# Kernel tuning notes

Measured on AMD Instinct MI355X. Metric: run time of the kernel, lower is better.

Reference implementation:

```python
import jax, jax.numpy as jnp
import numpy as np

N = 50000      # nodes
E = 600000     # edges (avg degree 12)
IN, H, OUT = 128, 256, 256


def setup_inputs() -> dict:
    key = jax.random.key(0)
    ks = jax.random.split(key, 9)
    glorot = lambda k, shp: jax.random.uniform(
        k, shp, jnp.float32, -1.0, 1.0) * np.sqrt(6.0 / (shp[0] + shp[1]))
    return {
        "x": jax.random.normal(ks[0], (N, IN), jnp.float32),
        "src": jax.random.randint(ks[1], (E,), 0, N, jnp.int32),
        "dst": jax.random.randint(ks[2], (E,), 0, N, jnp.int32),
        "W_conv": glorot(ks[3], (IN, H)),
        "b_conv": jnp.zeros((H,), jnp.float32),
        "W_fc": glorot(ks[4], (H, H)),
        "b_fc": jax.random.uniform(ks[5], (H,), jnp.float32, -1, 1) / np.sqrt(H),
        "W_fc2": glorot(ks[6], (H, OUT)),
        "b_fc2": jax.random.uniform(ks[7], (OUT,), jnp.float32, -1, 1) / np.sqrt(OUT),
    }


def reference(x, src, dst, W_conv, b_conv, W_fc, b_fc, W_fc2, b_fc2):
    ones = jnp.ones((E,), x.dtype)
    # dgl GraphConv, norm='both': D_in^{-1/2} A D_out^{-1/2} X W + b
    deg_out = jax.ops.segment_sum(ones, src, num_segments=N)
    deg_in = jax.ops.segment_sum(ones, dst, num_segments=N)
    norm_src = jax.lax.rsqrt(jnp.maximum(deg_out, 1.0))  # [N]
    norm_dst = jax.lax.rsqrt(jnp.maximum(deg_in, 1.0))   # [N]
    feat = x * norm_src[:, None]                          # [N, IN]
    agg = jax.ops.segment_sum(feat[src], dst, num_segments=N)  # gather+scatter SpMM
    h = agg * norm_dst[:, None]
    h = h @ W_conv + b_conv                               # GraphConv weight+bias
    # num_nonl_layers == 2 branch
    h = jax.nn.relu(h) @ W_fc + b_fc
    h = jax.nn.relu(h) @ W_fc2 + b_fc2
    return h
```

## Files before the change

kernel.cpp:

```cpp
#include <hip/hip_runtime.h>

#define NN 50000
#define NE 600000
#define FIN 128
#define CAP 128

typedef __attribute__((ext_vector_type(8))) short bf16x8;
typedef __attribute__((ext_vector_type(4))) float f32x4;

__device__ __forceinline__ float bf2f(unsigned short u) {
    union { unsigned int i; float f; } v; v.i = ((unsigned int)u) << 16; return v.f;
}
__device__ __forceinline__ unsigned short f2bf(float f) {
    union { float f; unsigned int i; } v; v.f = f;
    return (unsigned short)((v.i + 0x7FFFu + ((v.i >> 16) & 1u)) >> 16);
}

__global__ __launch_bounds__(256)
void bin_kernel(const int* __restrict__ src, const int* __restrict__ dst,
                int* __restrict__ cnt_in, int* __restrict__ cnt_out,
                int* __restrict__ csr_src) {
    int e0 = (blockIdx.x * 256 + threadIdx.x) * 4;
    if (e0 >= NE) return;
    int4 s4 = *(const int4*)(src + e0);
    int4 d4 = *(const int4*)(dst + e0);
    int p;
    p = atomicAdd(&cnt_in[d4.x], 1); if (p < CAP) csr_src[d4.x * CAP + p] = s4.x;
    atomicAdd(&cnt_out[s4.x], 1);
    p = atomicAdd(&cnt_in[d4.y], 1); if (p < CAP) csr_src[d4.y * CAP + p] = s4.y;
    atomicAdd(&cnt_out[s4.y], 1);
    p = atomicAdd(&cnt_in[d4.z], 1); if (p < CAP) csr_src[d4.z * CAP + p] = s4.z;
    atomicAdd(&cnt_out[s4.z], 1);
    p = atomicAdd(&cnt_in[d4.w], 1); if (p < CAP) csr_src[d4.w * CAP + p] = s4.w;
    atomicAdd(&cnt_out[s4.w], 1);
}

__global__ __launch_bounds__(256)
void gather_kernel(const float* __restrict__ x, const int* __restrict__ csr_src,
                   const int* __restrict__ cnt_in, const int* __restrict__ cnt_out,
                   unsigned short* __restrict__ agg) {
    int tid  = threadIdx.x;
    int grp  = tid >> 5;
    int lane = tid & 31;
    int r = blockIdx.x * 8 + grp;
    if (r >= NN) return;
    int deg = cnt_in[r];
    float nd = rsqrtf(fmaxf((float)deg, 1.0f));
    int cnt = deg > CAP ? CAP : deg;
    const int* bucket = csr_src + (size_t)r * CAP;
    const float* xb = x + lane * 4;
    float4 acc = {0.f, 0.f, 0.f, 0.f};
    for (int j0 = 0; j0 < cnt; j0 += 32) {
        int c = cnt - j0; if (c > 32) c = 32;
        int sv = 0; float nsl = 0.f;
        if (lane < c) {
            sv  = bucket[j0 + lane];
            nsl = rsqrtf(fmaxf((float)cnt_out[sv], 1.0f));
        }
        for (int i = 0; i < c; ++i) {
            int   s  = __shfl(sv,  i, 32);
            float ns = __shfl(nsl, i, 32);
            float4 xv = *(const float4*)(xb + (size_t)s * FIN);
            acc.x += xv.x * ns; acc.y += xv.y * ns;
            acc.z += xv.z * ns; acc.w += xv.w * ns;
        }
    }
    unsigned short o[4];
    o[0] = f2bf(acc.x * nd); o[1] = f2bf(acc.y * nd);
    o[2] = f2bf(acc.z * nd); o[3] = f2bf(acc.w * nd);
    *(uint2*)(agg + (size_t)r * FIN + lane * 4) = *(const uint2*)o;
}

template<int K, bool RELU>
__global__ __launch_bounds__(256)
void gemm_kernel(const unsigned short* __restrict__ A,
                 const float* __restrict__ W, const float* __restrict__ bias,
                 unsigned short* __restrict__ Cb, float* __restrict__ Cf, int ML) {
    const int PITCH = K + 24;
    __shared__ short bsh[64 * PITCH];
    int tid  = threadIdx.x;
    int wave = tid >> 6, lane = tid & 63;
    int quad = lane >> 4, l16 = lane & 15;
    int n0 = blockIdx.y * 64;
    #pragma unroll
    for (int k0 = 0; k0 < K; k0 += 4) {
        int k = k0 + (tid >> 6);
        int c = tid & 63;
        bsh[c * PITCH + k] = (short)f2bf(W[(size_t)k * 256 + n0 + c]);
    }
    __syncthreads();

    int m0 = blockIdx.x * 64 + wave * 16;
    int arow = m0 + l16; if (arow >= ML) arow = ML - 1;
    const unsigned short* Ap = A + (size_t)arow * K + quad * 8;

    f32x4 acc0 = {0.f, 0.f, 0.f, 0.f};
    f32x4 acc1 = acc0, acc2 = acc0, acc3 = acc0;
    #pragma unroll
    for (int k0 = 0; k0 < K; k0 += 32) {
        bf16x8 a  = *(const bf16x8*)(Ap + k0);
        bf16x8 b0 = *(const bf16x8*)&bsh[( 0 + l16) * PITCH + quad * 8 + k0];
        bf16x8 b1 = *(const bf16x8*)&bsh[(16 + l16) * PITCH + quad * 8 + k0];
        bf16x8 b2 = *(const bf16x8*)&bsh[(32 + l16) * PITCH + quad * 8 + k0];
        bf16x8 b3 = *(const bf16x8*)&bsh[(48 + l16) * PITCH + quad * 8 + k0];
        acc0 = __builtin_amdgcn_mfma_f32_16x16x32_bf16(a, b0, acc0, 0, 0, 0);
        acc1 = __builtin_amdgcn_mfma_f32_16x16x32_bf16(a, b1, acc1, 0, 0, 0);
        acc2 = __builtin_amdgcn_mfma_f32_16x16x32_bf16(a, b2, acc2, 0, 0, 0);
        acc3 = __builtin_amdgcn_mfma_f32_16x16x32_bf16(a, b3, acc3, 0, 0, 0);
    }
    f32x4 accs[4] = {acc0, acc1, acc2, acc3};
    #pragma unroll
    for (int c = 0; c < 4; ++c) {
        int col = n0 + c * 16 + l16;
        float bv = bias[col];
        #pragma unroll
        for (int r = 0; r < 4; ++r) {
            int rr = m0 + quad * 4 + r;
            if (rr < ML) {
                float v = accs[c][r] + bv;
                if (RELU) Cb[(size_t)rr * 256 + col] = f2bf(fmaxf(v, 0.0f));
                else      Cf[(size_t)rr * 256 + col] = v;
            }
        }
    }
}


extern "C" void kernel_launch(void* const* d_in, const int* in_sizes, int n_in,
                              void* d_out, int out_size, void* d_ws, size_t ws_size,
                              hipStream_t stream) {
    const float* x      = (const float*)d_in[0];
    const int*   src    = (const int*)d_in[1];
    const int*   dst    = (const int*)d_in[2];
    const float* W_conv = (const float*)d_in[3];
    const float* b_conv = (const float*)d_in[4];
    const float* W_fc   = (const float*)d_in[5];
    const float* b_fc   = (const float*)d_in[6];
    const float* W_fc2  = (const float*)d_in[7];
    const float* b_fc2  = (const float*)d_in[8];
    float* out = (float*)d_out;

    unsigned short* agg = (unsigned short*)d_out;

    char* ob = (char*)d_out;
    int* csr_src = (int*)(ob + 16000000);

    char* ws = (char*)d_ws;
    int* cnt_out = (int*)(ws + 0);
    int* cnt_in  = (int*)(ws + 204800);

    size_t avail = (ws_size > 409728) ? ws_size - 409728 : 0;
    long long cap = (long long)(avail / 1024);
    int CH = (int)((cap / 64) * 64);
    if (CH < 64) CH = 64;
    if (CH > 50048) CH = 50048;
    unsigned short* h1 = (unsigned short*)(ws + 409728);
    unsigned short* h2 = h1 + (size_t)CH * 256;

    hipMemsetAsync(d_ws, 0, 409600, stream);

    bin_kernel<<<(NE / 4 + 255) / 256, 256, 0, stream>>>(src, dst, cnt_in, cnt_out,
                                                         csr_src);
    gather_kernel<<<(NN + 7) / 8, 256, 0, stream>>>(x, csr_src, cnt_in, cnt_out, agg);

    int nchunks = (NN + CH - 1) / CH;
    for (int ci = nchunks - 1; ci >= 0; --ci) {
        int base = ci * CH;
        int ml = NN - base; if (ml > CH) ml = CH;
        dim3 g((ml + 63) / 64, 4);
        gemm_kernel<128, true ><<<g, 256, 0, stream>>>(agg + (size_t)base * FIN,
                                                       W_conv, b_conv, h1, nullptr, ml);
        gemm_kernel<256, true ><<<g, 256, 0, stream>>>(h1, W_fc,  b_fc,  h2, nullptr, ml);
        gemm_kernel<256, false><<<g, 256, 0, stream>>>(h2, W_fc2, b_fc2, nullptr,
                                                       out + (size_t)base * 256, ml);
    }
}
```

Baseline: 284.4 us.

## Fuse three dense layers into one kernel keeping activations in shared memory

Replaces the three chunked GEMM launches with a single fused MLP kernel. Each block computes a 64-row tile through all three layers, keeping intermediate activations in LDS and double-buffering transposed bf16 weight slices. A separate prep kernel converts the weights to bf16 once. Because agg aliases the output buffer, rows are processed in descending chunks so later launches never overwrite agg rows that are still unread. The aim is to remove the intermediate global round-trips and the per-block weight conversion, at the cost of heavy LDS use (about 140KB per block), which limits occupancy, and several launches over shrinking row ranges.

```diff
diff --git a/kernel.cpp b/kernel.cpp
--- a/kernel.cpp
+++ b/kernel.cpp
@@ -4,13 +4,12 @@
 #define NE 600000
 #define FIN 128
 #define CAP 128
+#define PW 280
+#define PH 280
 
 typedef __attribute__((ext_vector_type(8))) short bf16x8;
 typedef __attribute__((ext_vector_type(4))) float f32x4;
 
-__device__ __forceinline__ float bf2f(unsigned short u) {
-    union { unsigned int i; float f; } v; v.i = ((unsigned int)u) << 16; return v.f;
-}
 __device__ __forceinline__ unsigned short f2bf(float f) {
     union { float f; unsigned int i; } v; v.f = f;
     return (unsigned short)((v.i + 0x7FFFu + ((v.i >> 16) & 1u)) >> 16);
@@ -71,55 +70,175 @@
     *(uint2*)(agg + (size_t)r * FIN + lane * 4) = *(const uint2*)o;
 }
 
-template<int K, bool RELU>
-__global__ __launch_bounds__(256)
-void gemm_kernel(const unsigned short* __restrict__ A,
-                 const float* __restrict__ W, const float* __restrict__ bias,
-                 unsigned short* __restrict__ Cb, float* __restrict__ Cf, int ML) {
-    const int PITCH = K + 24;
-    __shared__ short bsh[64 * PITCH];
-    int tid  = threadIdx.x;
+__global__ __launch_bounds__(256)
+void wprep_kernel(const float* __restrict__ Wc, const float* __restrict__ W1,
+                  const float* __restrict__ W2, unsigned short* __restrict__ o) {
+    int t = blockIdx.x * 256 + threadIdx.x;
+    if (t < 32768) {
+        int n = t >> 7, k = t & 127;
+        o[t] = f2bf(Wc[k * 256 + n]);
+    } else if (t < 98304) {
+        int i = t - 32768; int n = i >> 8, k = i & 255;
+        o[32768 + i] = f2bf(W1[k * 256 + n]);
+    } else if (t < 163840) {
+        int i = t - 98304; int n = i >> 8, k = i & 255;
+        o[98304 + i] = f2bf(W2[k * 256 + n]);
+    }
+}
+
+__global__ __launch_bounds__(256)
+void fused_mlp_kernel(const unsigned short* __restrict__ agg,
+                      const unsigned short* __restrict__ Wct,
+                      const unsigned short* __restrict__ W1t,
+                      const unsigned short* __restrict__ W2t,
+                      const float* __restrict__ bc,
+                      const float* __restrict__ b1,
+                      const float* __restrict__ b2,
+                      float* __restrict__ out,
+                      int rowLo, int rowHi) {
+    __shared__ short wshA[64 * PW];
+    __shared__ short wshB[64 * PW];
+    __shared__ short hsh1[64 * PH];
+    __shared__ short hsh2[64 * PH];
+    int tid = threadIdx.x;
     int wave = tid >> 6, lane = tid & 63;
     int quad = lane >> 4, l16 = lane & 15;
-    int n0 = blockIdx.y * 64;
+    int B0 = rowLo + blockIdx.x * 64;
+    int m0 = wave * 16;
+    int sc = tid >> 2, sq = tid & 3;
+
+    int arow = B0 + m0 + l16; if (arow >= NN) arow = NN - 1;
+    const unsigned short* Ap = agg + (size_t)arow * FIN + quad * 8;
+    bf16x8 a1f[4];
     #pragma unroll
-    for (int k0 = 0; k0 < K; k0 += 4) {
-        int k = k0 + (tid >> 6);
-        int c = tid & 63;
-        bsh[c * PITCH + k] = (short)f2bf(W[(size_t)k * 256 + n0 + c]);
-    }
-    __syncthreads();
-
-    int m0 = blockIdx.x * 64 + wave * 16;
-    int arow = m0 + l16; if (arow >= ML) arow = ML - 1;
-    const unsigned short* Ap = A + (size_t)arow * K + quad * 8;
-
-    f32x4 acc0 = {0.f, 0.f, 0.f, 0.f};
-    f32x4 acc1 = acc0, acc2 = acc0, acc3 = acc0;
-    #pragma unroll
-    for (int k0 = 0; k0 < K; k0 += 32) {
-        bf16x8 a  = *(const bf16x8*)(Ap + k0);
-        bf16x8 b0 = *(const bf16x8*)&bsh[( 0 + l16) * PITCH + quad * 8 + k0];
-        bf16x8 b1 = *(const bf16x8*)&bsh[(16 + l16) * PITCH + quad * 8 + k0];
-        bf16x8 b2 = *(const bf16x8*)&bsh[(32 + l16) * PITCH + quad * 8 + k0];
-        bf16x8 b3 = *(const bf16x8*)&bsh[(48 + l16) * PITCH + quad * 8 + k0];
-        acc0 = __builtin_amdgcn_mfma_f32_16x16x32_bf16(a, b0, acc0, 0, 0, 0);
-        acc1 = __builtin_amdgcn_mfma_f32_16x16x32_bf16(a, b1, acc1, 0, 0, 0);
-        acc2 = __builtin_amdgcn_mfma_f32_16x16x32_bf16(a, b2, acc2, 0, 0, 0);
-        acc3 = __builtin_amdgcn_mfma_f32_16x16x32_bf16(a, b3, acc3, 0, 0, 0);
-    }
-    f32x4 accs[4] = {acc0, acc1, acc2, acc3};
-    #pragma unroll
-    for (int c = 0; c < 4; ++c) {
-        int col = n0 + c * 16 + l16;
-        float bv = bias[col];
-        #pragma unroll
-        for (int r = 0; r < 4; ++r) {
-            int rr = m0 + quad * 4 + r;
-            if (rr < ML) {
-                float v = accs[c][r] + bv;
-                if (RELU) Cb[(size_t)rr * 256 + col] = f2bf(fmaxf(v, 0.0f));
-                else      Cf[(size_t)rr * 256 + col] = v;
+    for (int i = 0; i < 4; ++i) a1f[i] = *(const bf16x8*)(Ap + i * 32);
+
+    {
+        const unsigned short* g0 = Wct + (size_t)sc * 128 + sq * 32;
+        #pragma unroll
+        for (int j = 0; j < 4; ++j)
+            *(bf16x8*)&wshA[sc * PW + sq * 32 + j * 8] = *(const bf16x8*)(g0 + j * 8);
+    }
+    #pragma unroll 1
+    for (int p = 0; p < 4; ++p) {
+        __syncthreads();
+        if (p < 3) {
+            const unsigned short* g = Wct + (size_t)((p + 1) * 64 + sc) * 128 + sq * 32;
+            short* d = (p & 1) ? wshA : wshB;
+            #pragma unroll
+            for (int j = 0; j < 4; ++j)
+                *(bf16x8*)&d[sc * PW + sq * 32 + j * 8] = *(const bf16x8*)(g + j * 8);
+        }
+        short* wb = (p & 1) ? wshB : wshA;
+        f32x4 ac0 = {0.f,0.f,0.f,0.f}, ac1 = ac0, ac2 = ac0, ac3 = ac0;
+        #pragma unroll
+        for (int i = 0; i < 4; ++i) {
+            int k0 = i * 32;
+            bf16x8 b0 = *(const bf16x8*)&wb[( 0 + l16) * PW + quad * 8 + k0];
+            bf16x8 b1v = *(const bf16x8*)&wb[(16 + l16) * PW + quad * 8 + k0];
+            bf16x8 b2v = *(const bf16x8*)&wb[(32 + l16) * PW + quad * 8 + k0];
+            bf16x8 b3v = *(const bf16x8*)&wb[(48 + l16) * PW + quad * 8 + k0];
+            ac0 = __builtin_amdgcn_mfma_f32_16x16x32_bf16(a1f[i], b0,  ac0, 0, 0, 0);
+            ac1 = __builtin_amdgcn_mfma_f32_16x16x32_bf16(a1f[i], b1v, ac1, 0, 0, 0);
+            ac2 = __builtin_amdgcn_mfma_f32_16x16x32_bf16(a1f[i], b2v, ac2, 0, 0, 0);
+            ac3 = __builtin_amdgcn_mfma_f32_16x16x32_bf16(a1f[i], b3v, ac3, 0, 0, 0);
+        }
+        int n0 = p * 64;
+        f32x4 accs[4] = {ac0, ac1, ac2, ac3};
+        #pragma unroll
+        for (int c = 0; c < 4; ++c) {
+            float bv = bc[n0 + c * 16 + l16];
+            #pragma unroll
+            for (int r = 0; r < 4; ++r)
+                hsh1[(m0 + quad * 4 + r) * PH + n0 + c * 16 + l16] =
+                    (short)f2bf(fmaxf(accs[c][r] + bv, 0.0f));
+        }
+    }
+
+    {
+        const unsigned short* g0 = W1t + (size_t)sc * 256 + sq * 64;
+        #pragma unroll
+        for (int j = 0; j < 8; ++j)
+            *(bf16x8*)&wshA[sc * PW + sq * 64 + j * 8] = *(const bf16x8*)(g0 + j * 8);
+    }
+    #pragma unroll 1
+    for (int p = 0; p < 4; ++p) {
+        __syncthreads();
+        if (p < 3) {
+            const unsigned short* g = W1t + (size_t)((p + 1) * 64 + sc) * 256 + sq * 64;
+            short* d = (p & 1) ? wshA : wshB;
+            #pragma unroll
+            for (int j = 0; j < 8; ++j)
+                *(bf16x8*)&d[sc * PW + sq * 64 + j * 8] = *(const bf16x8*)(g + j * 8);
+        }
+        short* wb = (p & 1) ? wshB : wshA;
+        f32x4 ac0 = {0.f,0.f,0.f,0.f}, ac1 = ac0, ac2 = ac0, ac3 = ac0;
+        #pragma unroll
+        for (int i = 0; i < 8; ++i) {
+            int k0 = i * 32;
+            bf16x8 a  = *(const bf16x8*)&hsh1[(m0 + l16) * PH + quad * 8 + k0];
+            bf16x8 b0 = *(const bf16x8*)&wb[( 0 + l16) * PW + quad * 8 + k0];
+            bf16x8 b1v = *(const bf16x8*)&wb[(16 + l16) * PW + quad * 8 + k0];
+            bf16x8 b2v = *(const bf16x8*)&wb[(32 + l16) * PW + quad * 8 + k0];
+            bf16x8 b3v = *(const bf16x8*)&wb[(48 + l16) * PW + quad * 8 + k0];
+            ac0 = __builtin_amdgcn_mfma_f32_16x16x32_bf16(a, b0,  ac0, 0, 0, 0);
+            ac1 = __builtin_amdgcn_mfma_f32_16x16x32_bf16(a, b1v, ac1, 0, 0, 0);
+            ac2 = __builtin_amdgcn_mfma_f32_16x16x32_bf16(a, b2v, ac2, 0, 0, 0);
+            ac3 = __builtin_amdgcn_mfma_f32_16x16x32_bf16(a, b3v, ac3, 0, 0, 0);
+        }
+        int n0 = p * 64;
+        f32x4 accs[4] = {ac0, ac1, ac2, ac3};
+        #pragma unroll
+        for (int c = 0; c < 4; ++c) {
+            float bv = b1[n0 + c * 16 + l16];
+            #pragma unroll
+            for (int r = 0; r < 4; ++r)
+                hsh2[(m0 + quad * 4 + r) * PH + n0 + c * 16 + l16] =
+                    (short)f2bf(fmaxf(accs[c][r] + bv, 0.0f));
+        }
+    }
+
+    {
+        const unsigned short* g0 = W2t + (size_t)sc * 256 + sq * 64;
+        #pragma unroll
+        for (int j = 0; j < 8; ++j)
+            *(bf16x8*)&wshA[sc * PW + sq * 64 + j * 8] = *(const bf16x8*)(g0 + j * 8);
+    }
+    #pragma unroll 1
+    for (int p = 0; p < 4; ++p) {
+        __syncthreads();
+        if (p < 3) {
+            const unsigned short* g = W2t + (size_t)((p + 1) * 64 + sc) * 256 + sq * 64;
+            short* d = (p & 1) ? wshA : wshB;
+            #pragma unroll
+            for (int j = 0; j < 8; ++j)
+                *(bf16x8*)&d[sc * PW + sq * 64 + j * 8] = *(const bf16x8*)(g + j * 8);
+        }
+        short* wb = (p & 1) ? wshB : wshA;
+        f32x4 ac0 = {0.f,0.f,0.f,0.f}, ac1 = ac0, ac2 = ac0, ac3 = ac0;
+        #pragma unroll
+        for (int i = 0; i < 8; ++i) {
+            int k0 = i * 32;
+            bf16x8 a  = *(const bf16x8*)&hsh2[(m0 + l16) * PH + quad * 8 + k0];
+            bf16x8 b0 = *(const bf16x8*)&wb[( 0 + l16) * PW + quad * 8 + k0];
+            bf16x8 b1v = *(const bf16x8*)&wb[(16 + l16) * PW + quad * 8 + k0];
+            bf16x8 b2v = *(const bf16x8*)&wb[(32 + l16) * PW + quad * 8 + k0];
+            bf16x8 b3v = *(const bf16x8*)&wb[(48 + l16) * PW + quad * 8 + k0];
+            ac0 = __builtin_amdgcn_mfma_f32_16x16x32_bf16(a, b0,  ac0, 0, 0, 0);
+            ac1 = __builtin_amdgcn_mfma_f32_16x16x32_bf16(a, b1v, ac1, 0, 0, 0);
+            ac2 = __builtin_amdgcn_mfma_f32_16x16x32_bf16(a, b2v, ac2, 0, 0, 0);
+            ac3 = __builtin_amdgcn_mfma_f32_16x16x32_bf16(a, b3v, ac3, 0, 0, 0);
+        }
+        int n0 = p * 64;
+        f32x4 accs[4] = {ac0, ac1, ac2, ac3};
+        #pragma unroll
+        for (int c = 0; c < 4; ++c) {
+            int col = n0 + c * 16 + l16;
+            float bv = b2[col];
+            #pragma unroll
+            for (int r = 0; r < 4; ++r) {
+                int rr = B0 + m0 + quad * 4 + r;
+                if (rr < rowHi) out[(size_t)rr * 256 + col] = accs[c][r] + bv;
             }
         }
     }
@@ -148,30 +267,23 @@
     char* ws = (char*)d_ws;
     int* cnt_out = (int*)(ws + 0);
     int* cnt_in  = (int*)(ws + 204800);
-
-    size_t avail = (ws_size > 409728) ? ws_size - 409728 : 0;
-    long long cap = (long long)(avail / 1024);
-    int CH = (int)((cap / 64) * 64);
-    if (CH < 64) CH = 64;
-    if (CH > 50048) CH = 50048;
-    unsigned short* h1 = (unsigned short*)(ws + 409728);
-    unsigned short* h2 = h1 + (size_t)CH * 256;
+    unsigned short* Wct = (unsigned short*)(ws + 0);
+    unsigned short* W1t = (unsigned short*)(ws + 65536);
+    unsigned short* W2t = (unsigned short*)(ws + 196608);
 
     hipMemsetAsync(d_ws, 0, 409600, stream);
 
     bin_kernel<<<(NE / 4 + 255) / 256, 256, 0, stream>>>(src, dst, cnt_in, cnt_out,
                                                          csr_src);
     gather_kernel<<<(NN + 7) / 8, 256, 0, stream>>>(x, csr_src, cnt_in, cnt_out, agg);
-
-    int nchunks = (NN + CH - 1) / CH;
-    for (int ci = nchunks - 1; ci >= 0; --ci) {
-        int base = ci * CH;
-        int ml = NN - base; if (ml > CH) ml = CH;
-        dim3 g((ml + 63) / 64, 4);
-        gemm_kernel<128, true ><<<g, 256, 0, stream>>>(agg + (size_t)base * FIN,
-                                                       W_conv, b_conv, h1, nullptr, ml);
-        gemm_kernel<256, true ><<<g, 256, 0, stream>>>(h1, W_fc,  b_fc,  h2, nullptr, ml);
-        gemm_kernel<256, false><<<g, 256, 0, stream>>>(h2, W_fc2, b_fc2, nullptr,
-                                                       out + (size_t)base * 256, ml);
-    }
-}
+    wprep_kernel<<<640, 256, 0, stream>>>(W_conv, W_fc, W_fc2, (unsigned short*)ws);
+
+    int hi = NN;
+    while (hi > 0) {
+        int lo = (hi <= 64) ? 0 : (hi + 3) / 4;
+        int nb = (hi - lo + 63) / 64;
+        fused_mlp_kernel<<<nb, 256, 0, stream>>>(agg, Wct, W1t, W2t,
+                                                 b_conv, b_fc, b_fc2, out, lo, hi);
+        hi = lo;
+    }
+}
```

Result: slower. 401.1 us (+41.0%).
